# Performance work log

Measured on AMD Instinct MI355X. Metric: run time of the kernel, lower is better.

## Reference

```python
import jax, jax.numpy as jnp
import numpy as np

B, S = 32, 4096
HID, MEM, ATT = 512, 512, 512


def setup_inputs() -> dict:
    key = jax.random.key(0)
    k1, k2, k3, k4, k5, k6, k7 = jax.random.split(key, 7)
    scale_h = 1.0 / np.sqrt(HID)
    scale_m = 1.0 / np.sqrt(MEM)
    scale_a = 1.0 / np.sqrt(ATT)
    return {
        "hidden": jax.random.normal(k1, (B, HID), dtype=jnp.float32),
        "memory": jax.random.normal(k2, (B, S, MEM), dtype=jnp.float32),
        "mem_pad": jnp.zeros((B, S), dtype=jnp.bool_),
        "coverage": jax.random.uniform(k3, (B, S), dtype=jnp.float32),
        # params stored as (in, out) so x @ W == torch Linear(x)
        "W_h": jax.random.uniform(k4, (HID, ATT), minval=-scale_h, maxval=scale_h, dtype=jnp.float32),
        "W_m": jax.random.uniform(k5, (MEM, ATT), minval=-scale_m, maxval=scale_m, dtype=jnp.float32),
        "W_c": jax.random.uniform(k6, (ATT,), minval=-1.0, maxval=1.0, dtype=jnp.float32),
        "v": jax.random.uniform(k7, (ATT,), minval=-scale_a, maxval=scale_a, dtype=jnp.float32),
    }


def reference(hidden, memory, mem_pad, coverage, W_h, W_m, W_c, v):
    h = hidden @ W_h                                   # (B, A)
    m = jnp.einsum('bsd,da->bsa', memory, W_m)         # (B, S, A)
    c_feat = coverage[..., None] * W_c                 # (B, S, A) ; Linear(1->A) == scalar * weight row
    score = jnp.einsum('bsa,a->bs', jnp.tanh(h[:, None, :] + m + c_feat), v)  # (B, S)
    score = jnp.where(mem_pad, -jnp.inf, score)
    attn_weights = jax.nn.softmax(score, axis=-1)      # (B, S)
    context = jnp.einsum('bs,bsd->bd', attn_weights, memory)  # (B, D)
    return context, attn_weights
```

## Files before the change

### kernel.cpp

```cpp
#include <hip/hip_runtime.h>
#include <hip/hip_bf16.h>
#include <math.h>

#define BB 32
#define SS 4096
#define DMEM 512
#define DATT 512

typedef short short8 __attribute__((ext_vector_type(8)));
typedef short short4v __attribute__((ext_vector_type(4)));
typedef float floatx4 __attribute__((ext_vector_type(4)));

__device__ inline short f2bf(float x) {
    unsigned u = __float_as_uint(x);
    unsigned r = (u + 0x7fffu + ((u >> 16) & 1u)) >> 16;
    return (short)(r & 0xffffu);
}

__device__ inline float fast_tanh(float x) {
    float e = __expf(2.0f * x);
    return 1.0f - 2.0f / (e + 1.0f);
}

__device__ inline void gld_lds16(const void* g, void* l) {
    __builtin_amdgcn_global_load_lds(
        (const __attribute__((address_space(1))) unsigned int*)g,
        (__attribute__((address_space(3))) unsigned int*)l, 16, 0, 0);
}


__global__ __launch_bounds__(256)
void conv_mem_kernel(const float* __restrict__ m, short* __restrict__ o) {
    size_t i = (size_t)blockIdx.x * 256 + threadIdx.x;
    const float4* p = (const float4*)m + i * 2;
    float4 a = p[0], b = p[1];
    short8 s;
    s[0] = f2bf(a.x); s[1] = f2bf(a.y); s[2] = f2bf(a.z); s[3] = f2bf(a.w);
    s[4] = f2bf(b.x); s[5] = f2bf(b.y); s[6] = f2bf(b.z); s[7] = f2bf(b.w);
    *((short8*)o + i) = s;
}

__global__ void prep_wt_kernel(const float* __restrict__ Wm, short* __restrict__ Wt) {
    const int n0 = blockIdx.x * 32;
    const int k0 = blockIdx.y * 32;
    const int t = threadIdx.x;
    const int r = t >> 5, c = t & 31;
    __shared__ float lds[32 * 33];
#pragma unroll
    for (int j = 0; j < 4; ++j) {
        int kk = r + j * 8;
        lds[kk * 33 + c] = Wm[(size_t)(k0 + kk) * 512 + n0 + c];
    }
    __syncthreads();
#pragma unroll
    for (int j = 0; j < 4; ++j) {
        int nn = r + j * 8;
        Wt[(size_t)(n0 + nn) * 512 + k0 + c] = f2bf(lds[c * 33 + nn]);
    }
}

__global__ void prep_h_kernel(const float* __restrict__ hidden, const float* __restrict__ Wh,
                              float* __restrict__ h) {
    const int b = blockIdx.x;
    const int n = blockIdx.y * 256 + threadIdx.x;
    const int kc = blockIdx.z;
    float acc = 0.f;
#pragma unroll 8
    for (int k = kc * 128; k < kc * 128 + 128; ++k)
        acc += hidden[b * 512 + k] * Wh[(size_t)k * 512 + n];
    atomicAdd(&h[b * 512 + n], acc);
}


__global__ __launch_bounds__(256, 3)
void score_kernel(const short* __restrict__ memB,
                  const float* __restrict__ coverage,
                  const short* __restrict__ Wt,
                  const float* __restrict__ h,
                  const float* __restrict__ Wc,
                  const float* __restrict__ v,
                  float* __restrict__ scores) {
    const int n0 = blockIdx.x * 128;
    const int s0 = blockIdx.y * 128;
    const int b  = blockIdx.z;
    const int tid = threadIdx.x;
    const int lane = tid & 63;
    const int wave = tid >> 6;
    const int wm = wave & 1;
    const int wn = wave >> 1;
    const int col = lane & 15;
    const int q = lane >> 4;

    __shared__ __align__(16) short tileA[128 * 64];
    __shared__ __align__(16) short tileB[128 * 64];
    __shared__ float covS[128];
    __shared__ float sred[2][128];

    if (tid < 128) covS[tid] = coverage[(size_t)b * SS + s0 + tid];

    const int srow = tid >> 3;
    const int gchunk = ((tid & 7) ^ (srow & 7)) * 16;
    const char* gA = (const char*)(memB + ((size_t)b * SS + s0) * 512);
    const char* gB = (const char*)(Wt + (size_t)n0 * 512);
    char* ldsAw = (char*)tileA + wave * 1024;
    char* ldsBw = (char*)tileB + wave * 1024;

    floatx4 acc[4][4];
#pragma unroll
    for (int mi = 0; mi < 4; ++mi)
#pragma unroll
        for (int ni = 0; ni < 4; ++ni)
            acc[mi][ni] = (floatx4){0.f, 0.f, 0.f, 0.f};

    for (int kt = 0; kt < 8; ++kt) {
        __syncthreads();
#pragma unroll
        for (int it = 0; it < 4; ++it) {
            size_t grow = (size_t)(it * 32 + srow) * 1024 + kt * 128 + gchunk;
            gld_lds16(gA + grow, ldsAw + it * 4096);
            gld_lds16(gB + grow, ldsBw + it * 4096);
        }
        __syncthreads();

#pragma unroll
        for (int ks = 0; ks < 2; ++ks) {
            short8 af[4], bf[4];
            const int ck = ks * 4 + q;
#pragma unroll
            for (int mi = 0; mi < 4; ++mi) {
                int row = wm * 64 + mi * 16 + col;
                af[mi] = *(const short8*)((const char*)tileA + row * 128 + ((ck ^ (col & 7)) * 16));
            }
#pragma unroll
            for (int ni = 0; ni < 4; ++ni) {
                int row = wn * 64 + ni * 16 + col;
                bf[ni] = *(const short8*)((const char*)tileB + row * 128 + ((ck ^ (col & 7)) * 16));
            }
#pragma unroll
            for (int mi = 0; mi < 4; ++mi)
#pragma unroll
                for (int ni = 0; ni < 4; ++ni)
                    acc[mi][ni] = __builtin_amdgcn_mfma_f32_16x16x32_bf16(af[mi], bf[ni], acc[mi][ni], 0, 0, 0);
        }
    }

    float hv[4], wcv[4], vv[4];
#pragma unroll
    for (int ni = 0; ni < 4; ++ni) {
        int n = n0 + wn * 64 + ni * 16 + col;
        hv[ni] = h[b * 512 + n];
        wcv[ni] = Wc[n];
        vv[ni] = v[n];
    }
    float rowAcc[4][4];
#pragma unroll
    for (int mi = 0; mi < 4; ++mi)
#pragma unroll
        for (int r = 0; r < 4; ++r)
            rowAcc[mi][r] = 0.f;
#pragma unroll
    for (int mi = 0; mi < 4; ++mi) {
#pragma unroll
        for (int r = 0; r < 4; ++r) {
            float cv = covS[wm * 64 + mi * 16 + q * 4 + r];
#pragma unroll
            for (int ni = 0; ni < 4; ++ni) {
                float val = acc[mi][ni][r] + hv[ni] + cv * wcv[ni];
                rowAcc[mi][r] += fast_tanh(val) * vv[ni];
            }
        }
    }
#pragma unroll
    for (int off = 1; off < 16; off <<= 1)
#pragma unroll
        for (int mi = 0; mi < 4; ++mi)
#pragma unroll
            for (int r = 0; r < 4; ++r)
                rowAcc[mi][r] += __shfl_xor(rowAcc[mi][r], off, 64);

    if (col == 0) {
#pragma unroll
        for (int mi = 0; mi < 4; ++mi)
#pragma unroll
            for (int r = 0; r < 4; ++r)
                sred[wn][wm * 64 + mi * 16 + q * 4 + r] = rowAcc[mi][r];
    }
    __syncthreads();
    if (tid < 128)
        atomicAdd(&scores[(size_t)b * SS + s0 + tid], sred[0][tid] + sred[1][tid]);
}

#define LDAF 72
__global__ __launch_bounds__(256, 2)
void score_fallback(const float* __restrict__ memory,
                    const float* __restrict__ coverage,
                    const short* __restrict__ Wt,
                    const float* __restrict__ h,
                    const float* __restrict__ Wc,
                    const float* __restrict__ v,
                    float* __restrict__ scores) {
    const int n0 = blockIdx.x * 128;
    const int s0 = blockIdx.y * 128;
    const int b  = blockIdx.z;
    const int tid = threadIdx.x;
    const int lane = tid & 63;
    const int wave = tid >> 6;
    const int wm = wave & 1;
    const int wn = wave >> 1;
    const int col = lane & 15;
    const int q = lane >> 4;

    __shared__ __align__(16) short tileA[128 * LDAF];
    __shared__ __align__(16) short tileB[128 * LDAF];
    __shared__ float covS[128];
    __shared__ float sred[2][128];

    if (tid < 128) covS[tid] = coverage[(size_t)b * SS + s0 + tid];

    floatx4 acc[4][4];
#pragma unroll
    for (int mi = 0; mi < 4; ++mi)
#pragma unroll
        for (int ni = 0; ni < 4; ++ni)
            acc[mi][ni] = (floatx4){0.f, 0.f, 0.f, 0.f};

    const float4* gA = (const float4*)(memory + ((size_t)b * SS + s0) * DMEM);
    const short*  gB = Wt + (size_t)n0 * 512;

    for (int kt = 0; kt < 8; ++kt) {
        __syncthreads();
#pragma unroll
        for (int it = 0; it < 8; ++it) {
            int i = tid + it * 256;
            int row = i >> 4, c4 = i & 15;
            float4 f = gA[row * 128 + kt * 16 + c4];
            short4v sv;
            sv.x = f2bf(f.x); sv.y = f2bf(f.y); sv.z = f2bf(f.z); sv.w = f2bf(f.w);
            *(short4v*)&tileA[row * LDAF + c4 * 4] = sv;
        }
#pragma unroll
        for (int it = 0; it < 4; ++it) {
            int i = tid + it * 256;
            int row = i >> 3, g = i & 7;
            short8 s = *(const short8*)(gB + (size_t)row * 512 + kt * 64 + g * 8);
            *(short8*)&tileB[row * LDAF + g * 8] = s;
        }
        __syncthreads();
#pragma unroll
        for (int ks = 0; ks < 2; ++ks) {
            short8 af[4], bf[4];
#pragma unroll
            for (int mi = 0; mi < 4; ++mi)
                af[mi] = *(const short8*)&tileA[(wm * 64 + mi * 16 + col) * LDAF + ks * 32 + q * 8];
#pragma unroll
            for (int ni = 0; ni < 4; ++ni)
                bf[ni] = *(const short8*)&tileB[(wn * 64 + ni * 16 + col) * LDAF + ks * 32 + q * 8];
#pragma unroll
            for (int mi = 0; mi < 4; ++mi)
#pragma unroll
                for (int ni = 0; ni < 4; ++ni)
                    acc[mi][ni] = __builtin_amdgcn_mfma_f32_16x16x32_bf16(af[mi], bf[ni], acc[mi][ni], 0, 0, 0);
        }
    }

    float hv[4], wcv[4], vv[4];
#pragma unroll
    for (int ni = 0; ni < 4; ++ni) {
        int n = n0 + wn * 64 + ni * 16 + col;
        hv[ni] = h[b * 512 + n];
        wcv[ni] = Wc[n];
        vv[ni] = v[n];
    }
    float rowAcc[4][4];
#pragma unroll
    for (int mi = 0; mi < 4; ++mi)
#pragma unroll
        for (int r = 0; r < 4; ++r)
            rowAcc[mi][r] = 0.f;
#pragma unroll
    for (int mi = 0; mi < 4; ++mi)
#pragma unroll
        for (int r = 0; r < 4; ++r) {
            float cv = covS[wm * 64 + mi * 16 + q * 4 + r];
#pragma unroll
            for (int ni = 0; ni < 4; ++ni) {
                float val = acc[mi][ni][r] + hv[ni] + cv * wcv[ni];
                rowAcc[mi][r] += fast_tanh(val) * vv[ni];
            }
        }
#pragma unroll
    for (int off = 1; off < 16; off <<= 1)
#pragma unroll
        for (int mi = 0; mi < 4; ++mi)
#pragma unroll
            for (int r = 0; r < 4; ++r)
                rowAcc[mi][r] += __shfl_xor(rowAcc[mi][r], off, 64);
    if (col == 0)
#pragma unroll
        for (int mi = 0; mi < 4; ++mi)
#pragma unroll
            for (int r = 0; r < 4; ++r)
                sred[wn][wm * 64 + mi * 16 + q * 4 + r] = rowAcc[mi][r];
    __syncthreads();
    if (tid < 128)
        atomicAdd(&scores[(size_t)b * SS + s0 + tid], sred[0][tid] + sred[1][tid]);
}

__global__ void softmax_kernel(const float* __restrict__ scores,
                               const unsigned char* __restrict__ pad,
                               float* __restrict__ attn_out) {
    const int b = blockIdx.x;
    const int tid = threadIdx.x;
    const int wave = tid >> 6, lane = tid & 63;
    __shared__ float redMax[16];
    __shared__ float redSum[16];

    float vals[4];
    float mx = -INFINITY;
#pragma unroll
    for (int i = 0; i < 4; ++i) {
        int idx = tid + i * 1024;
        float s = scores[(size_t)b * SS + idx];
        if (pad[(size_t)b * SS + idx]) s = -INFINITY;
        vals[i] = s;
        mx = fmaxf(mx, s);
    }
#pragma unroll
    for (int off = 32; off >= 1; off >>= 1) mx = fmaxf(mx, __shfl_xor(mx, off, 64));
    if (lane == 0) redMax[wave] = mx;
    __syncthreads();
    float gmax = -INFINITY;
#pragma unroll
    for (int w = 0; w < 16; ++w) gmax = fmaxf(gmax, redMax[w]);

    float sum = 0.f;
#pragma unroll
    for (int i = 0; i < 4; ++i) {
        float e = __expf(vals[i] - gmax);
        vals[i] = e;
        sum += e;
    }
#pragma unroll
    for (int off = 32; off >= 1; off >>= 1) sum += __shfl_xor(sum, off, 64);
    if (lane == 0) redSum[wave] = sum;
    __syncthreads();
    float gsum = 0.f;
#pragma unroll
    for (int w = 0; w < 16; ++w) gsum += redSum[w];
    const float inv = 1.0f / gsum;
#pragma unroll
    for (int i = 0; i < 4; ++i)
        attn_out[(size_t)b * SS + tid + i * 1024] = vals[i] * inv;
}

__global__ __launch_bounds__(256)
void context_kernel(const float* __restrict__ memory,
                    const float* __restrict__ attn,
                    float* __restrict__ ctx) {
    const int sc = blockIdx.x;
    const int dh = blockIdx.y;
    const int b  = blockIdx.z;
    const int t = threadIdx.x;
    const int c = t & 63;
    const int r = t >> 6;

    __shared__ float wS[128];
    __shared__ float4 red[3][64];

    if (t < 128) wS[t] = attn[(size_t)b * SS + sc * 128 + t];
    __syncthreads();

    const float4* m4 = (const float4*)(memory + ((size_t)b * SS + sc * 128) * DMEM) + dh * 64 + c;
    float4 acc = {0.f, 0.f, 0.f, 0.f};
#pragma unroll 8
    for (int i = 0; i < 32; ++i) {
        int row = i * 4 + r;
        float w = wS[row];
        float4 f = m4[(size_t)row * 128];
        acc.x += w * f.x; acc.y += w * f.y; acc.z += w * f.z; acc.w += w * f.w;
    }
    if (r > 0) red[r - 1][c] = acc;
    __syncthreads();
    if (r == 0) {
#pragma unroll
        for (int j = 0; j < 3; ++j) {
            float4 o = red[j][c];
            acc.x += o.x; acc.y += o.y; acc.z += o.z; acc.w += o.w;
        }
        float* dst = &ctx[b * 512 + dh * 256 + c * 4];
        atomicAdd(dst + 0, acc.x);
        atomicAdd(dst + 1, acc.y);
        atomicAdd(dst + 2, acc.z);
        atomicAdd(dst + 3, acc.w);
    }
}

extern "C" void kernel_launch(void* const* d_in, const int* in_sizes, int n_in,
                              void* d_out, int out_size, void* d_ws, size_t ws_size,
                              hipStream_t stream) {
    (void)in_sizes; (void)n_in; (void)out_size;
    const float* hidden   = (const float*)d_in[0];
    const float* memory   = (const float*)d_in[1];
    const unsigned char* mem_pad = (const unsigned char*)d_in[2];
    const float* coverage = (const float*)d_in[3];
    const float* Wh       = (const float*)d_in[4];
    const float* Wm       = (const float*)d_in[5];
    const float* Wc       = (const float*)d_in[6];
    const float* v        = (const float*)d_in[7];

    const size_t memB_bytes = (size_t)BB * SS * DMEM * 2;
    const size_t need = memB_bytes + 512 * 1024 + 64 * 1024 + 512 * 1024;
    char* ws = (char*)d_ws;

    float* ctx  = (float*)d_out;
    float* attn = (float*)d_out + BB * 512;

    if (ws_size >= need) {
        short* memB   = (short*)ws;
        short* Wt     = (short*)(ws + memB_bytes);
        float* h      = (float*)(ws + memB_bytes + 512 * 1024);
        float* scores = (float*)(ws + memB_bytes + 576 * 1024);

        hipMemsetAsync(ctx, 0, BB * 512 * sizeof(float), stream);
        hipMemsetAsync(h, 0, BB * 512 * sizeof(float), stream);
        hipMemsetAsync(scores, 0, BB * SS * sizeof(float), stream);
        conv_mem_kernel<<<dim3(BB * SS * DMEM / 8 / 256), dim3(256), 0, stream>>>(memory, memB);
        prep_wt_kernel<<<dim3(16, 16), dim3(256), 0, stream>>>(Wm, Wt);
        prep_h_kernel<<<dim3(32, 2, 4), dim3(256), 0, stream>>>(hidden, Wh, h);
        score_kernel<<<dim3(4, 32, 32), dim3(256), 0, stream>>>(memB, coverage, Wt, h, Wc, v, scores);
        softmax_kernel<<<dim3(BB), dim3(1024), 0, stream>>>(scores, mem_pad, attn);
        context_kernel<<<dim3(32, 2, BB), dim3(256), 0, stream>>>(memory, attn, ctx);
    } else {
        short* Wt     = (short*)ws;
        float* h      = (float*)(ws + 512 * 1024);
        float* scores = (float*)(ws + 576 * 1024);

        hipMemsetAsync(ctx, 0, BB * 512 * sizeof(float), stream);
        hipMemsetAsync(h, 0, BB * 512 * sizeof(float), stream);
        hipMemsetAsync(scores, 0, BB * SS * sizeof(float), stream);
        prep_wt_kernel<<<dim3(16, 16), dim3(256), 0, stream>>>(Wm, Wt);
        prep_h_kernel<<<dim3(32, 2, 4), dim3(256), 0, stream>>>(hidden, Wh, h);
        score_fallback<<<dim3(4, 32, 32), dim3(256), 0, stream>>>(memory, coverage, Wt, h, Wc, v, scores);
        softmax_kernel<<<dim3(BB), dim3(1024), 0, stream>>>(scores, mem_pad, attn);
        context_kernel<<<dim3(32, 2, BB), dim3(256), 0, stream>>>(memory, attn, ctx);
    }
}
```

Before: 547.2 us.

## Widen score tile to 256 attention columns and replace atomics with partial buffers

The score kernel now uses 512-thread blocks covering 256 attention columns instead of 128, halving the N-split so each memory tile is loaded from global twice rather than four times. Per-column-tile partial scores are written to two separate buffers that the softmax sums, replacing atomicAdd and the scores memset. prep_h now does the full K loop per thread with a plain store, dropping its memset and atomics. The larger blocks raise LDS and register pressure per block, which may reduce occupancy.

```diff
diff --git a/kernel.cpp b/kernel.cpp
--- a/kernel.cpp
+++ b/kernel.cpp
@@ -63,23 +63,150 @@
                               float* __restrict__ h) {
     const int b = blockIdx.x;
     const int n = blockIdx.y * 256 + threadIdx.x;
-    const int kc = blockIdx.z;
     float acc = 0.f;
 #pragma unroll 8
-    for (int k = kc * 128; k < kc * 128 + 128; ++k)
+    for (int k = 0; k < 512; ++k)
         acc += hidden[b * 512 + k] * Wh[(size_t)k * 512 + n];
-    atomicAdd(&h[b * 512 + n], acc);
-}
-
-
-__global__ __launch_bounds__(256, 3)
+    h[b * 512 + n] = acc;
+}
+
+
+__global__ __launch_bounds__(512, 4)
 void score_kernel(const short* __restrict__ memB,
                   const float* __restrict__ coverage,
                   const short* __restrict__ Wt,
                   const float* __restrict__ h,
                   const float* __restrict__ Wc,
                   const float* __restrict__ v,
-                  float* __restrict__ scores) {
+                  float* __restrict__ scoreParts) {
+    const int nt = blockIdx.x;
+    const int n0 = nt * 256;
+    const int s0 = blockIdx.y * 128;
+    const int b  = blockIdx.z;
+    const int tid = threadIdx.x;
+    const int lane = tid & 63;
+    const int wave = tid >> 6;
+    const int wm = wave & 1;
+    const int wn = wave >> 1;
+    const int col = lane & 15;
+    const int q = lane >> 4;
+
+    __shared__ __align__(16) short tileA[128 * 64];
+    __shared__ __align__(16) short tileB[256 * 64];
+    __shared__ float covS[128];
+    __shared__ float sred[4][128];
+
+    if (tid < 128) covS[tid] = coverage[(size_t)b * SS + s0 + tid];
+
+    const char* gA = (const char*)(memB + ((size_t)b * SS + s0) * 512);
+    const char* gB = (const char*)(Wt + (size_t)n0 * 512);
+    char* ldsA = (char*)tileA + wave * 1024;
+    char* ldsB = (char*)tileB + wave * 1024;
+
+    floatx4 acc[4][4];
+#pragma unroll
+    for (int mi = 0; mi < 4; ++mi)
+#pragma unroll
+        for (int ni = 0; ni < 4; ++ni)
+            acc[mi][ni] = (floatx4){0.f, 0.f, 0.f, 0.f};
+
+    for (int kt = 0; kt < 8; ++kt) {
+        __syncthreads();
+#pragma unroll
+        for (int it = 0; it < 2; ++it) {
+            int ci = it * 512 + tid;
+            int row = ci >> 3;
+            int gchunk = ((ci & 7) ^ (row & 7)) * 16;
+            gld_lds16(gA + (size_t)row * 1024 + kt * 128 + gchunk, ldsA + it * 8192);
+        }
+#pragma unroll
+        for (int it = 0; it < 4; ++it) {
+            int ci = it * 512 + tid;
+            int row = ci >> 3;
+            int gchunk = ((ci & 7) ^ (row & 7)) * 16;
+            gld_lds16(gB + (size_t)row * 1024 + kt * 128 + gchunk, ldsB + it * 8192);
+        }
+        __syncthreads();
+
+#pragma unroll
+        for (int ks = 0; ks < 2; ++ks) {
+            const int ck = ks * 4 + q;
+            const int sw = (ck ^ (col & 7)) * 16;
+            short8 af[4], bf[4];
+#pragma unroll
+            for (int mi = 0; mi < 4; ++mi) {
+                int row = wm * 64 + mi * 16 + col;
+                af[mi] = *(const short8*)((const char*)tileA + row * 128 + sw);
+            }
+#pragma unroll
+            for (int ni = 0; ni < 4; ++ni) {
+                int row = wn * 64 + ni * 16 + col;
+                bf[ni] = *(const short8*)((const char*)tileB + row * 128 + sw);
+            }
+#pragma unroll
+            for (int mi = 0; mi < 4; ++mi)
+#pragma unroll
+                for (int ni = 0; ni < 4; ++ni)
+                    acc[mi][ni] = __builtin_amdgcn_mfma_f32_16x16x32_bf16(af[mi], bf[ni], acc[mi][ni], 0, 0, 0);
+        }
+    }
+
+    float hv[4], wcv[4], vv[4];
+#pragma unroll
+    for (int ni = 0; ni < 4; ++ni) {
+        int n = n0 + wn * 64 + ni * 16 + col;
+        hv[ni] = h[b * 512 + n];
+        wcv[ni] = Wc[n];
+        vv[ni] = v[n];
+    }
+    float rowAcc[4][4];
+#pragma unroll
+    for (int mi = 0; mi < 4; ++mi)
+#pragma unroll
+        for (int r = 0; r < 4; ++r)
+            rowAcc[mi][r] = 0.f;
+#pragma unroll
+    for (int mi = 0; mi < 4; ++mi) {
+#pragma unroll
+        for (int r = 0; r < 4; ++r) {
+            float cv = covS[wm * 64 + mi * 16 + q * 4 + r];
+#pragma unroll
+            for (int ni = 0; ni < 4; ++ni) {
+                float val = acc[mi][ni][r] + hv[ni] + cv * wcv[ni];
+                rowAcc[mi][r] += fast_tanh(val) * vv[ni];
+            }
+        }
+    }
+#pragma unroll
+    for (int off = 1; off < 16; off <<= 1)
+#pragma unroll
+        for (int mi = 0; mi < 4; ++mi)
+#pragma unroll
+            for (int r = 0; r < 4; ++r)
+                rowAcc[mi][r] += __shfl_xor(rowAcc[mi][r], off, 64);
+
+    if (col == 0) {
+#pragma unroll
+        for (int mi = 0; mi < 4; ++mi)
+#pragma unroll
+            for (int r = 0; r < 4; ++r)
+                sred[wn][wm * 64 + mi * 16 + q * 4 + r] = rowAcc[mi][r];
+    }
+    __syncthreads();
+    if (tid < 128)
+        scoreParts[(size_t)nt * BB * SS + (size_t)b * SS + s0 + tid] =
+            sred[0][tid] + sred[1][tid] + sred[2][tid] + sred[3][tid];
+}
+
+#define LDAF 72
+__global__ __launch_bounds__(256, 2)
+void score_fallback(const float* __restrict__ memory,
+                    const float* __restrict__ coverage,
+                    const short* __restrict__ Wt,
+                    const float* __restrict__ h,
+                    const float* __restrict__ Wc,
+                    const float* __restrict__ v,
+                    float* __restrict__ scoreParts) {
     const int n0 = blockIdx.x * 128;
     const int s0 = blockIdx.y * 128;
     const int b  = blockIdx.z;
@@ -91,125 +218,6 @@
     const int col = lane & 15;
     const int q = lane >> 4;
 
-    __shared__ __align__(16) short tileA[128 * 64];
-    __shared__ __align__(16) short tileB[128 * 64];
-    __shared__ float covS[128];
-    __shared__ float sred[2][128];
-
-    if (tid < 128) covS[tid] = coverage[(size_t)b * SS + s0 + tid];
-
-    const int srow = tid >> 3;
-    const int gchunk = ((tid & 7) ^ (srow & 7)) * 16;
-    const char* gA = (const char*)(memB + ((size_t)b * SS + s0) * 512);
-    const char* gB = (const char*)(Wt + (size_t)n0 * 512);
-    char* ldsAw = (char*)tileA + wave * 1024;
-    char* ldsBw = (char*)tileB + wave * 1024;
-
-    floatx4 acc[4][4];
-#pragma unroll
-    for (int mi = 0; mi < 4; ++mi)
-#pragma unroll
-        for (int ni = 0; ni < 4; ++ni)
-            acc[mi][ni] = (floatx4){0.f, 0.f, 0.f, 0.f};
-
-    for (int kt = 0; kt < 8; ++kt) {
-        __syncthreads();
-#pragma unroll
-        for (int it = 0; it < 4; ++it) {
-            size_t grow = (size_t)(it * 32 + srow) * 1024 + kt * 128 + gchunk;
-            gld_lds16(gA + grow, ldsAw + it * 4096);
-            gld_lds16(gB + grow, ldsBw + it * 4096);
-        }
-        __syncthreads();
-
-#pragma unroll
-        for (int ks = 0; ks < 2; ++ks) {
-            short8 af[4], bf[4];
-            const int ck = ks * 4 + q;
-#pragma unroll
-            for (int mi = 0; mi < 4; ++mi) {
-                int row = wm * 64 + mi * 16 + col;
-                af[mi] = *(const short8*)((const char*)tileA + row * 128 + ((ck ^ (col & 7)) * 16));
-            }
-#pragma unroll
-            for (int ni = 0; ni < 4; ++ni) {
-                int row = wn * 64 + ni * 16 + col;
-                bf[ni] = *(const short8*)((const char*)tileB + row * 128 + ((ck ^ (col & 7)) * 16));
-            }
-#pragma unroll
-            for (int mi = 0; mi < 4; ++mi)
-#pragma unroll
-                for (int ni = 0; ni < 4; ++ni)
-                    acc[mi][ni] = __builtin_amdgcn_mfma_f32_16x16x32_bf16(af[mi], bf[ni], acc[mi][ni], 0, 0, 0);
-        }
-    }
-
-    float hv[4], wcv[4], vv[4];
-#pragma unroll
-    for (int ni = 0; ni < 4; ++ni) {
-        int n = n0 + wn * 64 + ni * 16 + col;
-        hv[ni] = h[b * 512 + n];
-        wcv[ni] = Wc[n];
-        vv[ni] = v[n];
-    }
-    float rowAcc[4][4];
-#pragma unroll
-    for (int mi = 0; mi < 4; ++mi)
-#pragma unroll
-        for (int r = 0; r < 4; ++r)
-            rowAcc[mi][r] = 0.f;
-#pragma unroll
-    for (int mi = 0; mi < 4; ++mi) {
-#pragma unroll
-        for (int r = 0; r < 4; ++r) {
-            float cv = covS[wm * 64 + mi * 16 + q * 4 + r];
-#pragma unroll
-            for (int ni = 0; ni < 4; ++ni) {
-                float val = acc[mi][ni][r] + hv[ni] + cv * wcv[ni];
-                rowAcc[mi][r] += fast_tanh(val) * vv[ni];
-            }
-        }
-    }
-#pragma unroll
-    for (int off = 1; off < 16; off <<= 1)
-#pragma unroll
-        for (int mi = 0; mi < 4; ++mi)
-#pragma unroll
-            for (int r = 0; r < 4; ++r)
-                rowAcc[mi][r] += __shfl_xor(rowAcc[mi][r], off, 64);
-
-    if (col == 0) {
-#pragma unroll
-        for (int mi = 0; mi < 4; ++mi)
-#pragma unroll
-            for (int r = 0; r < 4; ++r)
-                sred[wn][wm * 64 + mi * 16 + q * 4 + r] = rowAcc[mi][r];
-    }
-    __syncthreads();
-    if (tid < 128)
-        atomicAdd(&scores[(size_t)b * SS + s0 + tid], sred[0][tid] + sred[1][tid]);
-}
-
-#define LDAF 72
-__global__ __launch_bounds__(256, 2)
-void score_fallback(const float* __restrict__ memory,
-                    const float* __restrict__ coverage,
-                    const short* __restrict__ Wt,
-                    const float* __restrict__ h,
-                    const float* __restrict__ Wc,
-                    const float* __restrict__ v,
-                    float* __restrict__ scores) {
-    const int n0 = blockIdx.x * 128;
-    const int s0 = blockIdx.y * 128;
-    const int b  = blockIdx.z;
-    const int tid = threadIdx.x;
-    const int lane = tid & 63;
-    const int wave = tid >> 6;
-    const int wm = wave & 1;
-    const int wn = wave >> 1;
-    const int col = lane & 15;
-    const int q = lane >> 4;
-
     __shared__ __align__(16) short tileA[128 * LDAF];
     __shared__ __align__(16) short tileB[128 * LDAF];
     __shared__ float covS[128];
@@ -303,10 +311,10 @@
                 sred[wn][wm * 64 + mi * 16 + q * 4 + r] = rowAcc[mi][r];
     __syncthreads();
     if (tid < 128)
-        atomicAdd(&scores[(size_t)b * SS + s0 + tid], sred[0][tid] + sred[1][tid]);
-}
-
-__global__ void softmax_kernel(const float* __restrict__ scores,
+        atomicAdd(&scoreParts[(size_t)b * SS + s0 + tid], sred[0][tid] + sred[1][tid]);
+}
+
+__global__ void softmax_kernel(const float* __restrict__ scoreParts,
                                const unsigned char* __restrict__ pad,
                                float* __restrict__ attn_out) {
     const int b = blockIdx.x;
@@ -319,9 +327,9 @@
     float mx = -INFINITY;
 #pragma unroll
     for (int i = 0; i < 4; ++i) {
-        int idx = tid + i * 1024;
-        float s = scores[(size_t)b * SS + idx];
-        if (pad[(size_t)b * SS + idx]) s = -INFINITY;
+        size_t idx = (size_t)b * SS + tid + i * 1024;
+        float s = scoreParts[idx] + scoreParts[(size_t)BB * SS + idx];
+        if (pad[idx]) s = -INFINITY;
         vals[i] = s;
         mx = fmaxf(mx, s);
     }
@@ -409,39 +417,37 @@
     const float* v        = (const float*)d_in[7];
 
     const size_t memB_bytes = (size_t)BB * SS * DMEM * 2;
-    const size_t need = memB_bytes + 512 * 1024 + 64 * 1024 + 512 * 1024;
+    const size_t parts_bytes = (size_t)2 * BB * SS * sizeof(float);
+    const size_t need = memB_bytes + 512 * 1024 + 64 * 1024 + parts_bytes;
     char* ws = (char*)d_ws;
 
     float* ctx  = (float*)d_out;
     float* attn = (float*)d_out + BB * 512;
 
+    hipMemsetAsync(ctx, 0, BB * 512 * sizeof(float), stream);
+
     if (ws_size >= need) {
-        short* memB   = (short*)ws;
-        short* Wt     = (short*)(ws + memB_bytes);
-        float* h      = (float*)(ws + memB_bytes + 512 * 1024);
-        float* scores = (float*)(ws + memB_bytes + 576 * 1024);
-
-        hipMemsetAsync(ctx, 0, BB * 512 * sizeof(float), stream);
-        hipMemsetAsync(h, 0, BB * 512 * sizeof(float), stream);
-        hipMemsetAsync(scores, 0, BB * SS * sizeof(float), stream);
+        short* memB  = (short*)ws;
+        short* Wt    = (short*)(ws + memB_bytes);
+        float* h     = (float*)(ws + memB_bytes + 512 * 1024);
+        float* parts = (float*)(ws + memB_bytes + 576 * 1024);
+
         conv_mem_kernel<<<dim3(BB * SS * DMEM / 8 / 256), dim3(256), 0, stream>>>(memory, memB);
         prep_wt_kernel<<<dim3(16, 16), dim3(256), 0, stream>>>(Wm, Wt);
-        prep_h_kernel<<<dim3(32, 2, 4), dim3(256), 0, stream>>>(hidden, Wh, h);
-        score_kernel<<<dim3(4, 32, 32), dim3(256), 0, stream>>>(memB, coverage, Wt, h, Wc, v, scores);
-        softmax_kernel<<<dim3(BB), dim3(1024), 0, stream>>>(scores, mem_pad, attn);
+        prep_h_kernel<<<dim3(32, 2), dim3(256), 0, stream>>>(hidden, Wh, h);
+        score_kernel<<<dim3(2, 32, 32), dim3(512), 0, stream>>>(memB, coverage, Wt, h, Wc, v, parts);
+        softmax_kernel<<<dim3(BB), dim3(1024), 0, stream>>>(parts, mem_pad, attn);
         context_kernel<<<dim3(32, 2, BB), dim3(256), 0, stream>>>(memory, attn, ctx);
     } else {
-        short* Wt     = (short*)ws;
-        float* h      = (float*)(ws + 512 * 1024);
-        float* scores = (float*)(ws + 576 * 1024);
-
-        hipMemsetAsync(ctx, 0, BB * 512 * sizeof(float), stream);
-        hipMemsetAsync(h, 0, BB * 512 * sizeof(float), stream);
-        hipMemsetAsync(scores, 0, BB * SS * sizeof(float), stream);
+        short* Wt    = (short*)ws;
+        float* h     = (float*)(ws + 512 * 1024);
+        float* parts = (float*)(ws + 576 * 1024);
+
+        hipMemsetAsync(parts, 0, parts_bytes, stream);
         prep_wt_kernel<<<dim3(16, 16), dim3(256), 0, stream>>>(Wm, Wt);
-        prep_h_kernel<<<dim3(32, 2, 4), dim3(256), 0, stream>>>(hidden, Wh, h);
-        score_fallback<<<dim3(4, 32, 32), dim3(256), 0, stream>>>(memory, coverage, Wt, h, Wc, v, scores);
-        softmax_kernel<<<dim3(BB), dim3(1024), 0, stream>>>(scores, mem_pad, attn);
+        prep_h_kernel<<<dim3(32, 2), dim3(256), 0, stream>>>(hidden, Wh, h);
+        score_fallback<<<dim3(4, 32, 32), dim3(256), 0, stream>>>(memory, coverage, Wt, h, Wc, v, parts);
+        softmax_kernel<<<dim3(BB), dim3(1024), 0, stream>>>(parts, mem_pad, attn);
         context_kernel<<<dim3(32, 2, BB), dim3(256), 0, stream>>>(memory, attn, ctx);
     }
 }
```

After: 568.7 us. 1.04x slower.
